# Kernel optimization log

Hardware: AMD Instinct MI355X
Metric: run time of the kernel (lower is better)

## Reference

```python
import jax, jax.numpy as jnp
import numpy as np

D_IN, H1, H2, H3 = 1024, 512, 256, 128  # embedding MLP dims
D_CBP = 2048                             # compact bilinear pooling output dim
H_C = 1024                               # comparator hidden dim
CLASSES = 10
B = 16384
SLOPE = 0.2  # LeakyReLU negative slope


def _lrelu(x):
    return jnp.where(x >= 0, x, SLOPE * x)


def _embed(x, W1, b1, W2, b2, W3, b3):
    x = _lrelu(x @ W1 + b1)
    x = _lrelu(x @ W2 + b2)
    x = _lrelu(x @ W3 + b3)
    return x  # [B, 128]


def setup_inputs() -> dict:
    key = jax.random.key(0)
    ks = jax.random.split(key, 16)

    def lin(k, fan_in, fan_out):
        bound = 1.0 / np.sqrt(fan_in)
        kw, kb = jax.random.split(k)
        W = jax.random.uniform(kw, (fan_in, fan_out), jnp.float32, -bound, bound)
        b = jax.random.uniform(kb, (fan_out,), jnp.float32, -bound, bound)
        return W, b

    W1, b1 = lin(ks[0], D_IN, H1)
    W2, b2 = lin(ks[1], H1, H2)
    W3, b3 = lin(ks[2], H2, H3)
    Wc1, bc1 = lin(ks[3], D_CBP, H_C)
    Wc2, bc2 = lin(ks[4], H_C, CLASSES)

    X = jax.random.normal(ks[5], (B, D_IN), jnp.float32)
    Centers = jax.random.normal(ks[6], (B, D_IN), jnp.float32)

    # count-sketch hashes (int constants) and +-1 signs (float buffers)
    h1 = jax.random.randint(ks[7], (H3,), 0, D_CBP, jnp.int32)
    h2 = jax.random.randint(ks[8], (H3,), 0, D_CBP, jnp.int32)
    s1 = jnp.sign(jax.random.normal(ks[9], (H3,), jnp.float32)) + (jax.random.normal(ks[9], (H3,)) == 0)
    s2 = jnp.sign(jax.random.normal(ks[10], (H3,), jnp.float32)) + (jax.random.normal(ks[10], (H3,)) == 0)

    return {"X": X, "Centers": Centers,
            "W1": W1, "b1": b1, "W2": W2, "b2": b2, "W3": W3, "b3": b3,
            "h1": h1, "s1": s1, "h2": h2, "s2": s2,
            "Wc1": Wc1, "bc1": bc1, "Wc2": Wc2, "bc2": bc2}


def _cbp(x, y, h1, s1, h2, s2):
    # count-sketch via tiny dense sketch matrices [128, 2048]
    M1 = jnp.zeros((H3, D_CBP), x.dtype).at[jnp.arange(H3), h1].set(s1)
    M2 = jnp.zeros((H3, D_CBP), y.dtype).at[jnp.arange(H3), h2].set(s2)
    sk1 = x @ M1  # [B, 2048]
    sk2 = y @ M2
    # circular convolution via real FFT
    return jnp.fft.irfft(jnp.fft.rfft(sk1, axis=-1) * jnp.fft.rfft(sk2, axis=-1), n=D_CBP, axis=-1)


def reference(X, Centers, W1, b1, W2, b2, W3, b3, h1, s1, h2, s2, Wc1, bc1, Wc2, bc2):
    ex = _embed(X, W1, b1, W2, b2, W3, b3)        # [B, 128]
    ec = _embed(Centers, W1, b1, W2, b2, W3, b3)  # [B, 128]
    cbp = _cbp(ex, ec, h1, s1, h2, s2)            # [B, 2048]
    z = _lrelu(cbp @ Wc1 + bc1)                   # [B, 1024]
    logits = z @ Wc2 + bc2                        # [B, classes]
    return jax.nn.softmax(logits, axis=1)
```

## Files before the change

kernel.cpp:

```cpp
#include <hip/hip_runtime.h>
#include <hip/hip_bf16.h>
#include <math.h>

#define BATCH   16384
#define D_IN    1024
#define H1_DIM  512
#define H2_DIM  256
#define H3_DIM  128
#define D_CBP   2048
#define H_C     1024
#define CLASSES 10
#define SLOPE   0.2f

#define NK_PAD  1088
#define NF      (2 * NK_PAD)

typedef short v8s __attribute__((ext_vector_type(8)));
typedef float v4f __attribute__((ext_vector_type(4)));
typedef unsigned short u16;
typedef unsigned int   u32;

__device__ __forceinline__ float b2f(unsigned short u) {
  return __uint_as_float(((unsigned)u) << 16);
}
__device__ __forceinline__ u16 f2b(float f) {
  __hip_bfloat16 h = __float2bfloat16(f);
  return __builtin_bit_cast(unsigned short, h);
}

__device__ __forceinline__ void g2l16(const void* g, void* l) {
  __builtin_amdgcn_global_load_lds(
      (const __attribute__((address_space(1))) void*)g,
      (__attribute__((address_space(3))) void*)l, 16, 0, 0);
}

template <int CMUL>
__global__ __launch_bounds__(256) void gemm_bf16_t(
    const u16* __restrict__ A,
    const u16* __restrict__ Bt,
    const float* __restrict__ bias,
    u16* __restrict__ C,
    int M, int N, int K, float slope)
{
  __shared__ __align__(16) short Asb[5][128 * 32];
  __shared__ __align__(16) short Bsb[5][128 * 32];

  const int tid  = threadIdx.x;
  const int wave = tid >> 6, lane = tid & 63;
  const int wm = wave >> 1, wn = wave & 1;
  const int u = lane & 15, quad = lane >> 4;

  const int nwg = gridDim.x * gridDim.y;
  int id = blockIdx.y * gridDim.x + blockIdx.x;
  if ((nwg & 7) == 0) id = (id & 7) * (nwg >> 3) + (id >> 3);
  const int m0 = (id / gridDim.x) * 128, n0 = (id % gridDim.x) * 128;

  const int g_log = ((lane & 3) - ((lane >> 3) & 3)) & 3;
  const int srow  = wave * 32 + (lane >> 2);
  const u16* gA0 = A  + (size_t)(m0 + srow)      * K + g_log * 8;
  const u16* gA1 = A  + (size_t)(m0 + srow + 16) * K + g_log * 8;
  const u16* gB0 = Bt + (size_t)(n0 + srow)      * K + g_log * 8;
  const u16* gB1 = Bt + (size_t)(n0 + srow + 16) * K + g_log * 8;
  const int lo0 = (wave * 32)      * 32;
  const int lo1 = (wave * 32 + 16) * 32;

  const int gran = (quad + (u >> 1)) & 3;
  int offA[4], offB[4];
#pragma unroll
  for (int i = 0; i < 4; ++i) {
    offA[i] = (wm * 64 + i * 16 + u) * 32 + gran * 8;
    offB[i] = (wn * 64 + i * 16 + u) * 32 + gran * 8;
  }

  v4f acc[4][4];
#pragma unroll
  for (int i = 0; i < 4; ++i)
#pragma unroll
    for (int j = 0; j < 4; ++j) acc[i][j] = (v4f){0.f, 0.f, 0.f, 0.f};

  const int nsteps = K >> 5;

  auto stage = [&](int s, int buf) {
    const int k0 = s * 32;
    g2l16(gA0 + k0, &Asb[buf][lo0]);
    g2l16(gA1 + k0, &Asb[buf][lo1]);
    g2l16(gB0 + k0, &Bsb[buf][lo0]);
    g2l16(gB1 + k0, &Bsb[buf][lo1]);
  };

  stage(0, 0);
  if (nsteps > 1) stage(1, 1);
  if (nsteps > 2) stage(2, 2);

  int cb = 0, sb = 3;
  for (int t = 0; t < nsteps; ++t) {
    if (t + 3 < nsteps) stage(t + 3, sb);

    const int rem = nsteps - 1 - t;
    if (rem >= 3)      asm volatile("s_waitcnt vmcnt(12)" ::: "memory");
    else if (rem == 2) asm volatile("s_waitcnt vmcnt(8)"  ::: "memory");
    else if (rem == 1) asm volatile("s_waitcnt vmcnt(4)"  ::: "memory");
    else               asm volatile("s_waitcnt vmcnt(0)"  ::: "memory");
    __builtin_amdgcn_s_barrier();
    asm volatile("" ::: "memory");

    v8s a[4], b[4];
#pragma unroll
    for (int i = 0; i < 4; ++i) a[i] = *(const v8s*)&Asb[cb][offA[i]];
#pragma unroll
    for (int j = 0; j < 4; ++j) b[j] = *(const v8s*)&Bsb[cb][offB[j]];
#pragma unroll
    for (int i = 0; i < 4; ++i)
#pragma unroll
      for (int j = 0; j < 4; ++j)
        acc[i][j] = __builtin_amdgcn_mfma_f32_16x16x32_bf16(a[i], b[j], acc[i][j], 0, 0, 0);

    cb = (cb == 4) ? 0 : cb + 1;
    sb = (sb == 4) ? 0 : sb + 1;
  }

  if (CMUL == 0) {
    float bcol[4];
#pragma unroll
    for (int j = 0; j < 4; ++j) bcol[j] = bias[n0 + wn * 64 + j * 16 + u];
#pragma unroll
    for (int i = 0; i < 4; ++i)
#pragma unroll
      for (int r = 0; r < 4; ++r) {
        const size_t ro = (size_t)(m0 + wm * 64 + i * 16 + quad * 4 + r) * N
                          + n0 + wn * 64 + u;
#pragma unroll
        for (int j = 0; j < 4; ++j) {
          float v = acc[i][j][r] + bcol[j];
          v = v >= 0.f ? v : slope * v;
          C[ro + j * 16] = f2b(v);
        }
      }
  } else {
    const bool im = (u & 1);
#pragma unroll
    for (int i = 0; i < 4; ++i)
#pragma unroll
      for (int r = 0; r < 4; ++r) {
        const size_t ro = (size_t)(m0 + wm * 64 + i * 16 + quad * 4 + r) * N
                          + n0 + wn * 64 + u;
#pragma unroll
        for (int j = 0; j < 4; ++j) {
          const float f2v = acc[i][j][r];
          const float f2p = __shfl_xor(f2v, 1, 64);
          const float f1v = b2f(C[ro + j * 16]);
          const float f1p = __shfl_xor(f1v, 1, 64);
          const float outv = im ? (f1p * f2v + f1v * f2p)
                                : (f1v * f2v - f1p * f2p);
          C[ro + j * 16] = f2b(outv);
        }
      }
  }
}

#define CAST_NB (BATCH * D_IN / 4 / 256)
__global__ __launch_bounds__(256) void cast2_bf16(
    const float* __restrict__ srcA, const float* __restrict__ srcB,
    u16* __restrict__ dst)
{
  const int bx = blockIdx.x;
  const float* s = (bx < CAST_NB) ? srcA : srcB;
  const int i = ((bx < CAST_NB) ? bx : bx - CAST_NB) * 256 + threadIdx.x;
  u16* d = dst + ((bx < CAST_NB) ? 0 : (size_t)BATCH * D_IN);
  const float4 v = ((const float4*)s)[i];
  __align__(8) u16 o[4] = {f2b(v.x), f2b(v.y), f2b(v.z), f2b(v.w)};
  *(uint2*)(d + (size_t)i * 4) = *(uint2*)o;
}

__global__ __launch_bounds__(256) void transpose_cast4(
    const float* __restrict__ W1, u16* __restrict__ W1t,
    const float* __restrict__ W2, u16* __restrict__ W2t,
    const float* __restrict__ W3, u16* __restrict__ W3t,
    const float* __restrict__ Wc1, u16* __restrict__ Wc1t)
{
  __shared__ float tile[32][33];
  const int z = blockIdx.z;
  const float* W; u16* Wt; int K, N;
  if      (z == 0) { W = W1;  Wt = W1t;  K = D_IN;   N = H1_DIM; }
  else if (z == 1) { W = W2;  Wt = W2t;  K = H1_DIM; N = H2_DIM; }
  else if (z == 2) { W = W3;  Wt = W3t;  K = H2_DIM; N = H3_DIM; }
  else             { W = Wc1; Wt = Wc1t; K = D_CBP;  N = H_C;    }
  const int k0 = blockIdx.x * 32, n0 = blockIdx.y * 32;
  if (k0 >= K || n0 >= N) return;
  const int tx = threadIdx.x & 31, ty = threadIdx.x >> 5;
#pragma unroll
  for (int s = 0; s < 4; ++s) {
    const int k = ty * 4 + s;
    tile[k][tx] = W[(size_t)(k0 + k) * N + n0 + tx];
  }
  __syncthreads();
#pragma unroll
  for (int s = 0; s < 4; ++s) {
    const int n = ty * 4 + s;
    Wt[(size_t)(n0 + n) * K + k0 + tx] = f2b(tile[tx][n]);
  }
}


__global__ __launch_bounds__(256) void setup_tab(
    float2* __restrict__ tab, float* __restrict__ zbias)
{
  const int t = blockIdx.x * 256 + threadIdx.x;
  if (t < D_CBP) {
    const float ang = 6.2831853071795864769f * (float)t / (float)D_CBP;
    tab[t] = make_float2(__cosf(ang), __sinf(ang));
  }
  if (t < NF) zbias[t] = 0.f;
}

__global__ __launch_bounds__(256) void gen_C(
    const float2* __restrict__ tab,
    const int* __restrict__ h1, const float* __restrict__ s1,
    const int* __restrict__ h2, const float* __restrict__ s2,
    u16* __restrict__ C1t, u16* __restrict__ C2t)
{
  const int id = blockIdx.x * 256 + threadIdx.x;
  if (id >= NF * H3_DIM) return;
  const int m = id >> 7, i = id & 127;
  const int k = m >> 1;
  float v1 = 0.f, v2 = 0.f;
  if (m < 2 * (D_CBP / 2 + 1)) {
    const float2 c1 = tab[(k * h1[i]) & (D_CBP - 1)];
    const float2 c2 = tab[(k * h2[i]) & (D_CBP - 1)];
    v1 = (m & 1) ? -s1[i] * c1.y : s1[i] * c1.x;
    v2 = (m & 1) ? -s2[i] * c2.y : s2[i] * c2.x;
  }
  C1t[id] = f2b(v1);
  C2t[id] = f2b(v2);
}

__global__ __launch_bounds__(256) void gen_T(
    const float2* __restrict__ tab, u16* __restrict__ Tt)
{
  const int id = blockIdx.x * 256 + threadIdx.x;
  const int m = id >> 8, q0 = (id & 255) * 8;
  const int k = m >> 1;
  const float sc = ((k == 0) || (k == D_CBP / 2)) ? (1.f / D_CBP) : (2.f / D_CBP);
  __align__(16) u16 o[8];
#pragma unroll
  for (int j = 0; j < 8; ++j) {
    float v = 0.f;
    if (m < 2 * (D_CBP / 2 + 1)) {
      const float2 cs = tab[(k * (q0 + j)) & (D_CBP - 1)];
      v = (m & 1) ? -sc * cs.y : sc * cs.x;
    }
    o[j] = f2b(v);
  }
  *(v8s*)&Tt[(size_t)m * D_CBP + q0] = *(v8s*)o;
}

__global__ __launch_bounds__(256) void head_softmax(
    const u16* __restrict__ Z, const float* __restrict__ Wc2,
    const float* __restrict__ bc2, float* __restrict__ out)
{
  const int row  = blockIdx.x * 4 + (threadIdx.x >> 6);
  const int lane = threadIdx.x & 63;

  float acc[CLASSES];
#pragma unroll
  for (int c = 0; c < CLASSES; ++c) acc[c] = 0.f;

  const u16* z = Z + (size_t)row * H_C;
  for (int k = lane; k < H_C; k += 64) {
    const float zv = b2f(z[k]);
    const float* w = Wc2 + (size_t)k * CLASSES;
#pragma unroll
    for (int c = 0; c < CLASSES; ++c) acc[c] += zv * w[c];
  }
#pragma unroll
  for (int c = 0; c < CLASSES; ++c) {
#pragma unroll
    for (int off = 32; off > 0; off >>= 1)
      acc[c] += __shfl_down(acc[c], off);
  }
  if (lane == 0) {
    float l[CLASSES], mx = -1e30f;
#pragma unroll
    for (int c = 0; c < CLASSES; ++c) { l[c] = acc[c] + bc2[c]; mx = fmaxf(mx, l[c]); }
    float s = 0.f;
#pragma unroll
    for (int c = 0; c < CLASSES; ++c) { l[c] = __expf(l[c] - mx); s += l[c]; }
    const float inv = 1.f / s;
#pragma unroll
    for (int c = 0; c < CLASSES; ++c) out[(size_t)row * CLASSES + c] = l[c] * inv;
  }
}

extern "C" void kernel_launch(void* const* d_in, const int* in_sizes, int n_in,
                              void* d_out, int out_size, void* d_ws, size_t ws_size,
                              hipStream_t stream) {
  const float* X       = (const float*)d_in[0];
  const float* Centers = (const float*)d_in[1];
  const float* W1      = (const float*)d_in[2];
  const float* b1      = (const float*)d_in[3];
  const float* W2      = (const float*)d_in[4];
  const float* b2      = (const float*)d_in[5];
  const float* W3      = (const float*)d_in[6];
  const float* b3      = (const float*)d_in[7];
  const int*   h1      = (const int*)d_in[8];
  const float* s1      = (const float*)d_in[9];
  const int*   h2      = (const int*)d_in[10];
  const float* s2      = (const float*)d_in[11];
  const float* Wc1     = (const float*)d_in[12];
  const float* bc1     = (const float*)d_in[13];
  const float* Wc2     = (const float*)d_in[14];
  const float* bc2     = (const float*)d_in[15];
  float* out = (float*)d_out;

  char* ws = (char*)d_ws;
  const size_t MB = 1u << 20;
  const size_t KB = 1u << 10;
  u16*    Xb    = (u16*)(ws);
  u16*    Tt    = (u16*)(ws);
  u16*    FWt   = (u16*)(ws + 8 * MB + 512 * KB);
  u16*    F1    = (u16*)(ws + 13 * MB);
  u16*    E1b   = (u16*)(ws + 64 * MB);
  u16*    Zb    = (u16*)(ws + 81 * MB);
  u16*    E2b   = (u16*)(ws + 96 * MB);
  u16*    E3b   = (u16*)(ws + 113 * MB);
  u16*    W1t   = (u16*)(ws + 121 * MB);
  u16*    W2t   = (u16*)(ws + 122 * MB);
  u16*    W3t   = (u16*)(ws + 122 * MB + 256 * KB);
  u16*    Wc1t  = (u16*)(ws + 122 * MB + 512 * KB);
  u16*    C1t   = (u16*)(ws + 126 * MB + 512 * KB);
  u16*    C2t   = (u16*)(ws + 127 * MB + 64 * KB);
  float2* tab   = (float2*)(ws + 127 * MB + 640 * KB);
  float*  zbias = (float*)(ws + 127 * MB + 672 * KB);

  const dim3 blk(256);

  cast2_bf16<<<dim3(2 * CAST_NB), blk, 0, stream>>>(X, Centers, Xb);

  transpose_cast4<<<dim3(D_CBP / 32, H_C / 32, 4), blk, 0, stream>>>(
      W1, W1t, W2, W2t, W3, W3t, Wc1, Wc1t);

  setup_tab<<<dim3(9), blk, 0, stream>>>(tab, zbias);
  gen_C<<<dim3(NF * H3_DIM / 256), blk, 0, stream>>>(tab, h1, s1, h2, s2, C1t, C2t);

  gemm_bf16_t<0><<<dim3(H1_DIM / 128, 2 * BATCH / 128), blk, 0, stream>>>(
      Xb, W1t, b1, E1b, 2 * BATCH, H1_DIM, D_IN, SLOPE);

  gen_T<<<dim3(NF), blk, 0, stream>>>(tab, Tt);
  gemm_bf16_t<0><<<dim3(NF / 128, H_C / 128), blk, 0, stream>>>(
      Wc1t, Tt, zbias, FWt, H_C, NF, D_CBP, 1.0f);

  gemm_bf16_t<0><<<dim3(H2_DIM / 128, 2 * BATCH / 128), blk, 0, stream>>>(
      E1b, W2t, b2, E2b, 2 * BATCH, H2_DIM, H1_DIM, SLOPE);
  gemm_bf16_t<0><<<dim3(H3_DIM / 128, 2 * BATCH / 128), blk, 0, stream>>>(
      E2b, W3t, b3, E3b, 2 * BATCH, H3_DIM, H2_DIM, SLOPE);

  gemm_bf16_t<0><<<dim3(NF / 128, BATCH / 128), blk, 0, stream>>>(
      E3b, C1t, zbias, F1, BATCH, NF, H3_DIM, 1.0f);
  gemm_bf16_t<1><<<dim3(NF / 128, BATCH / 128), blk, 0, stream>>>(
      E3b + (size_t)BATCH * H3_DIM, C2t, zbias, F1, BATCH, NF, H3_DIM, 1.0f);
  gemm_bf16_t<0><<<dim3(H_C / 128, BATCH / 128), blk, 0, stream>>>(
      F1, FWt, bc1, Zb, BATCH, H_C, NF, SLOPE);

  head_softmax<<<dim3(BATCH / 4), blk, 0, stream>>>(Zb, Wc2, bc2, out);
}
```

Baseline: 517.1 us.

## Fuse both count-sketch spectrum GEMMs and complex multiply into one kernel

Replaces the two separate sketch-spectrum GEMM launches (the second reading back the first's bf16 output for the complex product) with a single kernel that computes both spectra into two register accumulators and does the complex multiply in registers before one store. This removes a full bf16 write plus read of the [B, 2176] intermediate and one launch, and also avoids the bf16 rounding of the first spectrum. It also adds separate leading-dimension arguments so the final comparator GEMM runs over only 2080 of the 2176 padded frequency columns, skipping padded K work. The cost is doubled accumulator registers in the fused kernel, which may lower occupancy.

```diff
diff --git a/kernel.cpp b/kernel.cpp
--- a/kernel.cpp
+++ b/kernel.cpp
@@ -14,6 +14,7 @@
 
 #define NK_PAD  1088
 #define NF      (2 * NK_PAD)
+#define NF_USED 2080
 
 typedef short v8s __attribute__((ext_vector_type(8)));
 typedef float v4f __attribute__((ext_vector_type(4)));
@@ -34,13 +35,12 @@
       (__attribute__((address_space(3))) void*)l, 16, 0, 0);
 }
 
-template <int CMUL>
-__global__ __launch_bounds__(256) void gemm_bf16_t(
+__global__ __launch_bounds__(256) void gemm_bf16(
     const u16* __restrict__ A,
     const u16* __restrict__ Bt,
     const float* __restrict__ bias,
     u16* __restrict__ C,
-    int M, int N, int K, float slope)
+    int M, int N, int K, int lda, int ldb, float slope)
 {
   __shared__ __align__(16) short Asb[5][128 * 32];
   __shared__ __align__(16) short Bsb[5][128 * 32];
@@ -57,10 +57,10 @@
 
   const int g_log = ((lane & 3) - ((lane >> 3) & 3)) & 3;
   const int srow  = wave * 32 + (lane >> 2);
-  const u16* gA0 = A  + (size_t)(m0 + srow)      * K + g_log * 8;
-  const u16* gA1 = A  + (size_t)(m0 + srow + 16) * K + g_log * 8;
-  const u16* gB0 = Bt + (size_t)(n0 + srow)      * K + g_log * 8;
-  const u16* gB1 = Bt + (size_t)(n0 + srow + 16) * K + g_log * 8;
+  const u16* gA0 = A  + (size_t)(m0 + srow)      * lda + g_log * 8;
+  const u16* gA1 = A  + (size_t)(m0 + srow + 16) * lda + g_log * 8;
+  const u16* gB0 = Bt + (size_t)(n0 + srow)      * ldb + g_log * 8;
+  const u16* gB1 = Bt + (size_t)(n0 + srow + 16) * ldb + g_log * 8;
   const int lo0 = (wave * 32)      * 32;
   const int lo1 = (wave * 32 + 16) * 32;
 
@@ -119,43 +119,130 @@
     sb = (sb == 4) ? 0 : sb + 1;
   }
 
-  if (CMUL == 0) {
-    float bcol[4];
-#pragma unroll
-    for (int j = 0; j < 4; ++j) bcol[j] = bias[n0 + wn * 64 + j * 16 + u];
+  float bcol[4];
+#pragma unroll
+  for (int j = 0; j < 4; ++j) bcol[j] = bias[n0 + wn * 64 + j * 16 + u];
+#pragma unroll
+  for (int i = 0; i < 4; ++i)
+#pragma unroll
+    for (int r = 0; r < 4; ++r) {
+      const size_t ro = (size_t)(m0 + wm * 64 + i * 16 + quad * 4 + r) * N
+                        + n0 + wn * 64 + u;
+#pragma unroll
+      for (int j = 0; j < 4; ++j) {
+        float v = acc[i][j][r] + bcol[j];
+        v = v >= 0.f ? v : slope * v;
+        C[ro + j * 16] = f2b(v);
+      }
+    }
+}
+
+__device__ __forceinline__ void f_pass(
+    const u16* gA0, const u16* gA1, const u16* gB0, const u16* gB1,
+    short (*Asb)[128 * 32], short (*Bsb)[128 * 32],
+    int lo0, int lo1, const int* offA, const int* offB,
+    v4f (&acc)[4][4])
+{
+  auto stage = [&](int s, int buf) {
+    const int k0 = s * 32;
+    g2l16(gA0 + k0, &Asb[buf][lo0]);
+    g2l16(gA1 + k0, &Asb[buf][lo1]);
+    g2l16(gB0 + k0, &Bsb[buf][lo0]);
+    g2l16(gB1 + k0, &Bsb[buf][lo1]);
+  };
+  stage(0, 0); stage(1, 1); stage(2, 2);
+#pragma unroll
+  for (int t = 0; t < 4; ++t) {
+    if (t == 0) stage(3, 3);
+    if (t == 0)      asm volatile("s_waitcnt vmcnt(12)" ::: "memory");
+    else if (t == 1) asm volatile("s_waitcnt vmcnt(8)"  ::: "memory");
+    else if (t == 2) asm volatile("s_waitcnt vmcnt(4)"  ::: "memory");
+    else             asm volatile("s_waitcnt vmcnt(0)"  ::: "memory");
+    __builtin_amdgcn_s_barrier();
+    asm volatile("" ::: "memory");
+    v8s a[4], b[4];
+#pragma unroll
+    for (int i = 0; i < 4; ++i) a[i] = *(const v8s*)&Asb[t][offA[i]];
+#pragma unroll
+    for (int j = 0; j < 4; ++j) b[j] = *(const v8s*)&Bsb[t][offB[j]];
 #pragma unroll
     for (int i = 0; i < 4; ++i)
 #pragma unroll
-      for (int r = 0; r < 4; ++r) {
-        const size_t ro = (size_t)(m0 + wm * 64 + i * 16 + quad * 4 + r) * N
-                          + n0 + wn * 64 + u;
-#pragma unroll
-        for (int j = 0; j < 4; ++j) {
-          float v = acc[i][j][r] + bcol[j];
-          v = v >= 0.f ? v : slope * v;
-          C[ro + j * 16] = f2b(v);
-        }
+      for (int j = 0; j < 4; ++j)
+        acc[i][j] = __builtin_amdgcn_mfma_f32_16x16x32_bf16(a[i], b[j], acc[i][j], 0, 0, 0);
+  }
+}
+
+__global__ __launch_bounds__(256) void gemm_f1f2(
+    const u16* __restrict__ E3,
+    const u16* __restrict__ C1t,
+    const u16* __restrict__ C2t,
+    u16* __restrict__ F1)
+{
+  __shared__ __align__(16) short Asb[5][128 * 32];
+  __shared__ __align__(16) short Bsb[5][128 * 32];
+
+  const int tid  = threadIdx.x;
+  const int wave = tid >> 6, lane = tid & 63;
+  const int wm = wave >> 1, wn = wave & 1;
+  const int u = lane & 15, quad = lane >> 4;
+  const int N = NF, K = H3_DIM;
+
+  const int nwg = gridDim.x * gridDim.y;
+  int id = blockIdx.y * gridDim.x + blockIdx.x;
+  if ((nwg & 7) == 0) id = (id & 7) * (nwg >> 3) + (id >> 3);
+  const int m0 = (id / gridDim.x) * 128, n0 = (id % gridDim.x) * 128;
+
+  const int g_log = ((lane & 3) - ((lane >> 3) & 3)) & 3;
+  const int srow  = wave * 32 + (lane >> 2);
+  const size_t aoffX = (size_t)(m0 + srow) * K + g_log * 8;
+  const size_t boff  = (size_t)(n0 + srow) * K + g_log * 8;
+  const int lo0 = (wave * 32)      * 32;
+  const int lo1 = (wave * 32 + 16) * 32;
+
+  const int gran = (quad + (u >> 1)) & 3;
+  int offA[4], offB[4];
+#pragma unroll
+  for (int i = 0; i < 4; ++i) {
+    offA[i] = (wm * 64 + i * 16 + u) * 32 + gran * 8;
+    offB[i] = (wn * 64 + i * 16 + u) * 32 + gran * 8;
+  }
+
+  v4f acc1[4][4], acc2[4][4];
+#pragma unroll
+  for (int i = 0; i < 4; ++i)
+#pragma unroll
+    for (int j = 0; j < 4; ++j) {
+      acc1[i][j] = (v4f){0.f, 0.f, 0.f, 0.f};
+      acc2[i][j] = (v4f){0.f, 0.f, 0.f, 0.f};
+    }
+
+  f_pass(E3 + aoffX, E3 + aoffX + (size_t)16 * K,
+         C1t + boff, C1t + boff + (size_t)16 * K,
+         Asb, Bsb, lo0, lo1, offA, offB, acc1);
+  const size_t aoffC = aoffX + (size_t)BATCH * K;
+  f_pass(E3 + aoffC, E3 + aoffC + (size_t)16 * K,
+         C2t + boff, C2t + boff + (size_t)16 * K,
+         Asb, Bsb, lo0, lo1, offA, offB, acc2);
+
+  const bool im = (u & 1);
+#pragma unroll
+  for (int i = 0; i < 4; ++i)
+#pragma unroll
+    for (int r = 0; r < 4; ++r) {
+      const size_t ro = (size_t)(m0 + wm * 64 + i * 16 + quad * 4 + r) * N
+                        + n0 + wn * 64 + u;
+#pragma unroll
+      for (int j = 0; j < 4; ++j) {
+        const float f1v = acc1[i][j][r];
+        const float f1p = __shfl_xor(f1v, 1, 64);
+        const float f2v = acc2[i][j][r];
+        const float f2p = __shfl_xor(f2v, 1, 64);
+        const float outv = im ? (f1p * f2v + f1v * f2p)
+                              : (f1v * f2v - f1p * f2p);
+        F1[ro + j * 16] = f2b(outv);
       }
-  } else {
-    const bool im = (u & 1);
-#pragma unroll
-    for (int i = 0; i < 4; ++i)
-#pragma unroll
-      for (int r = 0; r < 4; ++r) {
-        const size_t ro = (size_t)(m0 + wm * 64 + i * 16 + quad * 4 + r) * N
-                          + n0 + wn * 64 + u;
-#pragma unroll
-        for (int j = 0; j < 4; ++j) {
-          const float f2v = acc[i][j][r];
-          const float f2p = __shfl_xor(f2v, 1, 64);
-          const float f1v = b2f(C[ro + j * 16]);
-          const float f1p = __shfl_xor(f1v, 1, 64);
-          const float outv = im ? (f1p * f2v + f1v * f2p)
-                                : (f1v * f2v - f1p * f2p);
-          C[ro + j * 16] = f2b(outv);
-        }
-      }
-  }
+    }
 }
 
 #define CAST_NB (BATCH * D_IN / 4 / 256)
@@ -342,24 +429,23 @@
   setup_tab<<<dim3(9), blk, 0, stream>>>(tab, zbias);
   gen_C<<<dim3(NF * H3_DIM / 256), blk, 0, stream>>>(tab, h1, s1, h2, s2, C1t, C2t);
 
-  gemm_bf16_t<0><<<dim3(H1_DIM / 128, 2 * BATCH / 128), blk, 0, stream>>>(
-      Xb, W1t, b1, E1b, 2 * BATCH, H1_DIM, D_IN, SLOPE);
+  gemm_bf16<<<dim3(H1_DIM / 128, 2 * BATCH / 128), blk, 0, stream>>>(
+      Xb, W1t, b1, E1b, 2 * BATCH, H1_DIM, D_IN, D_IN, D_IN, SLOPE);
 
   gen_T<<<dim3(NF), blk, 0, stream>>>(tab, Tt);
-  gemm_bf16_t<0><<<dim3(NF / 128, H_C / 128), blk, 0, stream>>>(
-      Wc1t, Tt, zbias, FWt, H_C, NF, D_CBP, 1.0f);
-
-  gemm_bf16_t<0><<<dim3(H2_DIM / 128, 2 * BATCH / 128), blk, 0, stream>>>(
-      E1b, W2t, b2, E2b, 2 * BATCH, H2_DIM, H1_DIM, SLOPE);
-  gemm_bf16_t<0><<<dim3(H3_DIM / 128, 2 * BATCH / 128), blk, 0, stream>>>(
-      E2b, W3t, b3, E3b, 2 * BATCH, H3_DIM, H2_DIM, SLOPE);
-
-  gemm_bf16_t<0><<<dim3(NF / 128, BATCH / 128), blk, 0, stream>>>(
-      E3b, C1t, zbias, F1, BATCH, NF, H3_DIM, 1.0f);
-  gemm_bf16_t<1><<<dim3(NF / 128, BATCH / 128), blk, 0, stream>>>(
-      E3b + (size_t)BATCH * H3_DIM, C2t, zbias, F1, BATCH, NF, H3_DIM, 1.0f);
-  gemm_bf16_t<0><<<dim3(H_C / 128, BATCH / 128), blk, 0, stream>>>(
-      F1, FWt, bc1, Zb, BATCH, H_C, NF, SLOPE);
+  gemm_bf16<<<dim3(NF / 128, H_C / 128), blk, 0, stream>>>(
+      Wc1t, Tt, zbias, FWt, H_C, NF, D_CBP, D_CBP, D_CBP, 1.0f);
+
+  gemm_bf16<<<dim3(H2_DIM / 128, 2 * BATCH / 128), blk, 0, stream>>>(
+      E1b, W2t, b2, E2b, 2 * BATCH, H2_DIM, H1_DIM, H1_DIM, H1_DIM, SLOPE);
+  gemm_bf16<<<dim3(H3_DIM / 128, 2 * BATCH / 128), blk, 0, stream>>>(
+      E2b, W3t, b3, E3b, 2 * BATCH, H3_DIM, H2_DIM, H2_DIM, H2_DIM, SLOPE);
+
+  gemm_f1f2<<<dim3(NF / 128, BATCH / 128), blk, 0, stream>>>(
+      E3b, C1t, C2t, F1);
+
+  gemm_bf16<<<dim3(H_C / 128, BATCH / 128), blk, 0, stream>>>(
+      F1, FWt, bc1, Zb, BATCH, H_C, NF_USED, NF, NF, SLOPE);
 
   head_softmax<<<dim3(BATCH / 4), blk, 0, stream>>>(Zb, Wc2, bc2, out);
 }
```

After: 470.2 us. -9.1%, faster.
